# Optimization experiments

Hardware: AMD Instinct MI355X
Metric: run time of the kernel (lower is better)

The kernel has to match this reference:

```python
import jax, jax.numpy as jnp
import numpy as np

B, T, D, E = 2, 1653, 512, 8
D_E = D // E
BE = B * E


def setup_inputs() -> dict:
    key = jax.random.key(0)
    ks = jax.random.split(key, 11)
    s = 0.02  # keep linear-layer scale sane
    return {
        "input": jax.random.normal(ks[0], (B, T, D), jnp.float32),
        "Wq": jax.random.normal(ks[1], (D, D), jnp.float32) * s,
        "bq": jax.random.normal(ks[2], (D,), jnp.float32) * s,
        "Wk": jax.random.normal(ks[3], (D, D), jnp.float32) * s,
        "bk": jax.random.normal(ks[4], (D,), jnp.float32) * s,
        "Wv": jax.random.normal(ks[5], (D, D), jnp.float32) * s,
        "bv": jax.random.normal(ks[6], (D,), jnp.float32) * s,
        "Wo": jax.random.normal(ks[7], (D, D), jnp.float32) * s,
        "bo": jax.random.normal(ks[8], (D,), jnp.float32) * s,
        # random 'gaussian orthogonal punishment' matrix (diag(norms) @ blockwise-QR in torch; random here)
        "punish": jax.random.normal(ks[9], (T, T), jnp.float32) * (1.0 / np.sqrt(T)),
        # random tensor produced by torch.nn.init.orthogonal_(att_score) in the source
        "att_orth": jax.random.normal(ks[10], (BE, T, T), jnp.float32) * (1.0 / np.sqrt(T)),
    }


def _learnable_sigmoid(x):
    return 1.2 / (1.0 + jnp.exp(-1.6 * x))


def reference(input, Wq, bq, Wk, bk, Wv, bv, Wo, bo, punish, att_orth):
    # torch nn.Linear: y = x @ W^T + b
    def proj(W, b):
        # [B,T,D] -> permute(0,2,1) -> [B,D,T] -> reshape to [B*E, T, D_E]
        y = jnp.einsum('btd,ed->bte', input, W) + b
        return y.transpose(0, 2, 1).reshape(BE, T, D_E)

    Q = _learnable_sigmoid(proj(Wq, bq))            # [BE, T, D_E] (mask_q is all-ones => no-op)
    K = _learnable_sigmoid(proj(Wk, bk))            # [BE, T, D_E]
    V = proj(Wv, bv)                                # [BE, T, D_E]

    inv_sqrt_T = 1.0 / jnp.sqrt(jnp.float32(T))
    att = jnp.einsum('btd,bsd->bts', Q, K) * inv_sqrt_T  # [BE, T, T]

    # punishment: elementwise mul by broadcast punish matrix, then matmul with
    # the (transposed) random orthogonal tensor: att = (att * P) @ orth^T
    att = (att * punish[None, :, :]) @ att_orth.transpose(0, 2, 1)  # [BE, T, T]

    att = jnp.where(att == 0.0, jnp.float32(-2e20), att)  # masked_fill(att==0, -2e20)

    out = jnp.einsum('bts,bsd->btd', att, V)        # [BE, T, D_E]
    # permute(0,2,1) -> [BE, D_E, T] -> reshape [B, D, T] -> permute -> [B, T, D]
    out = out.transpose(0, 2, 1).reshape(B, D, T).transpose(0, 2, 1)
    return jnp.einsum('btd,ed->bte', out, Wo) + bo   # [B, T, D]
```

## Files before the change

### kernel.cpp

```cpp
#include <hip/hip_runtime.h>

#define TT 1653
#define DD 512
#define BB 2
#define DE 64
#define BEH 16
#define TTILES 26
#define TPAD 1664
#define SQN 26
#define NJC 4
#define MPSTRIDE TPAD

typedef __attribute__((ext_vector_type(8))) short bf16x8;
typedef __attribute__((ext_vector_type(4))) float f32x4;
typedef short bf16x8u __attribute__((ext_vector_type(8), aligned(4)));
typedef float f32x4u  __attribute__((ext_vector_type(4), aligned(4)));

__device__ __forceinline__ short f2bf(float f) {
    union { float f; unsigned u; } v; v.f = f;
    unsigned r = v.u + 0x7fffu + ((v.u >> 16) & 1u);
    return (short)(r >> 16);
}
__device__ __forceinline__ unsigned pack2(float a, float b) {
    return (unsigned)(unsigned short)f2bf(a) | ((unsigned)(unsigned short)f2bf(b) << 16);
}
__device__ __forceinline__ float bf2f(short s) {
    union { unsigned u; float f; } v; v.u = ((unsigned)(unsigned short)s) << 16;
    return v.f;
}
__device__ __forceinline__ bf16x8 ld_frag4(const short* p) {
    bf16x8u v = *(const bf16x8u*)p;
    return (bf16x8)v;
}

__device__ __forceinline__ void bar_fenced() {
    __builtin_amdgcn_sched_barrier(0);
    __builtin_amdgcn_s_barrier();
    __builtin_amdgcn_sched_barrier(0);
}
__device__ __forceinline__ void lgkm0_bar() {
    asm volatile("s_waitcnt lgkmcnt(0)" ::: "memory");
    __builtin_amdgcn_sched_barrier(0);
    __builtin_amdgcn_s_barrier();
    __builtin_amdgcn_sched_barrier(0);
}

__global__ __launch_bounds__(256) void projconv_kernel(
    const float* __restrict__ X,
    const float* __restrict__ W0, const float* __restrict__ b0,
    const float* __restrict__ W1, const float* __restrict__ b1,
    const float* __restrict__ W2, const float* __restrict__ b2,
    const float* __restrict__ P,
    short* __restrict__ Y0, short* __restrict__ Y1, short* __restrict__ Y2,
    short* __restrict__ Pbf)
{
    __shared__ __align__(16) short Wsh[64][72];
    __shared__ __align__(16) short Xs[64][72];

    const int tid = threadIdx.x;
    const int z = blockIdx.z;

    if (z == 6) {
        const int cid = blockIdx.x + TTILES * blockIdx.y;
        const int NG4 = TPAD / 4;
        for (int g = cid * 256 + tid; g < TT * NG4; g += 208 * 256) {
            const int r = g / NG4, c4 = (g - r * NG4) * 4;
            float p0 = 0.f, p1 = 0.f, p2 = 0.f, p3 = 0.f;
            const float* prow = P + (size_t)r * TT;
            if (c4 + 0 < TT) p0 = prow[c4 + 0];
            if (c4 + 1 < TT) p1 = prow[c4 + 1];
            if (c4 + 2 < TT) p2 = prow[c4 + 2];
            if (c4 + 3 < TT) p3 = prow[c4 + 3];
            uint2 o; o.x = pack2(p0, p1); o.y = pack2(p2, p3);
            *(uint2*)(Pbf + (size_t)r * TPAD + c4) = o;
        }
        return;
    }

    const int tt = blockIdx.x, dt = blockIdx.y;
    const int b = z / 3, which = z % 3;
    const float* W    = (which == 0) ? W0 : (which == 1) ? W1 : W2;
    const float* bias = (which == 0) ? b0 : (which == 1) ? b1 : b2;
    short* Y          = (which == 0) ? Y0 : (which == 1) ? Y1 : Y2;

    const int t0 = tt * 64, d0 = dt * 64;
    const float* Xb = X + (size_t)b * TT * DD;

    const int wave = tid >> 6, lane = tid & 63;
    const int quad = lane >> 4, l16 = lane & 15;
    const int srow = tid >> 2, scg = (tid & 3) * 16;
    const int trow = t0 + srow;
    const int rx = min(trow, TT - 1);

    f32x4 acc[4];
    #pragma unroll
    for (int i = 0; i < 4; ++i) acc[i] = (f32x4){0.f, 0.f, 0.f, 0.f};

    float4 w0, w1, w2, w3, x0, x1, x2, x3;

    auto stage = [&](int k0) {
        const float* wrow = W + (size_t)(d0 + srow) * DD + k0 + scg;
        w0 = *(const float4*)(wrow);
        w1 = *(const float4*)(wrow + 4);
        w2 = *(const float4*)(wrow + 8);
        w3 = *(const float4*)(wrow + 12);
        const float* xrow = Xb + (size_t)rx * DD + k0 + scg;
        x0 = *(const float4*)(xrow);
        x1 = *(const float4*)(xrow + 4);
        x2 = *(const float4*)(xrow + 8);
        x3 = *(const float4*)(xrow + 12);
    };
    auto lds_write = [&]() {
        const bool tv = (trow < TT);
        float4 zz = make_float4(0.f, 0.f, 0.f, 0.f);
        float4 y0 = tv ? x0 : zz, y1 = tv ? x1 : zz;
        float4 y2 = tv ? x2 : zz, y3 = tv ? x3 : zz;
        uint4 pw0, pw1, px0, px1;
        pw0.x = pack2(w0.x, w0.y); pw0.y = pack2(w0.z, w0.w);
        pw0.z = pack2(w1.x, w1.y); pw0.w = pack2(w1.z, w1.w);
        pw1.x = pack2(w2.x, w2.y); pw1.y = pack2(w2.z, w2.w);
        pw1.z = pack2(w3.x, w3.y); pw1.w = pack2(w3.z, w3.w);
        px0.x = pack2(y0.x, y0.y); px0.y = pack2(y0.z, y0.w);
        px0.z = pack2(y1.x, y1.y); px0.w = pack2(y1.z, y1.w);
        px1.x = pack2(y2.x, y2.y); px1.y = pack2(y2.z, y2.w);
        px1.z = pack2(y3.x, y3.y); px1.w = pack2(y3.z, y3.w);
        *(uint4*)&Wsh[srow][scg]     = pw0;
        *(uint4*)&Wsh[srow][scg + 8] = pw1;
        *(uint4*)&Xs[srow][scg]      = px0;
        *(uint4*)&Xs[srow][scg + 8]  = px1;
    };

    stage(0);
    for (int k0 = 0; k0 < DD; k0 += 64) {
        lds_write();
        if (k0 + 64 < DD) stage(k0 + 64);
        lgkm0_bar();

        #pragma unroll
        for (int ks = 0; ks < 2; ++ks) {
            bf16x8 a = *(const bf16x8*)&Wsh[wave * 16 + l16][ks * 32 + quad * 8];
            #pragma unroll
            for (int nt = 0; nt < 4; ++nt) {
                bf16x8 bb = *(const bf16x8*)&Xs[nt * 16 + l16][ks * 32 + quad * 8];
                acc[nt] = __builtin_amdgcn_mfma_f32_16x16x32_bf16(a, bb, acc[nt], 0, 0, 0);
            }
        }
        bar_fenced();
    }

    #pragma unroll
    for (int nt = 0; nt < 4; ++nt) {
        const int t = t0 + nt * 16 + l16;
        if (t < TT) {
            #pragma unroll
            for (int r = 0; r < 4; ++r) {
                const int d = d0 + wave * 16 + quad * 4 + r;
                float v = acc[nt][r] + bias[d];
                if (which < 2) v = 1.2f / (1.0f + __expf(-1.6f * v));
                Y[((size_t)b * DD + d) * TT + t] = f2bf(v);
            }
        }
    }
}

struct OVStage {
    f32x4u o0a, o0b, o1a, o1b;
    uint2  v0a, v0b, v1a, v1b;
};

__global__ __launch_bounds__(256) void ovt8_kernel(
    const float* __restrict__ orth, const short* __restrict__ Vb,
    float* __restrict__ Mpart)
{
    __shared__ __align__(16) short Os[64][70];
    __shared__ __align__(16) short Vs[64][70];

    const int flat = blockIdx.x + TTILES * (blockIdx.y + BEH * blockIdx.z);
    const int xcd = flat & 7;
    const int j8  = flat >> 3;
    const int sq  = j8 % 26;
    const int slice = xcd * 8 + (j8 / 26);
    const int be = slice & 15;
    const int jc = slice >> 4;

    const int s0 = sq * 64;
    const int jt0 = (jc < 2) ? jc * 7 : 14 + (jc - 2) * 6;
    const int jtn = (jc < 2) ? 7 : 6;

    const float* O  = orth + (size_t)be * TT * TT;
    const short* Vh = Vb + (size_t)be * DE * TT;

    const int tid  = threadIdx.x;
    const int wave = tid >> 6, lane = tid & 63;
    const int quad = lane >> 4, l16 = lane & 15;

    const int p  = tid >> 4;
    const int sc = tid & 15;
    const int ca = s0 + 4 * sc;
    const bool fastS = (s0 + 64 <= TT);

    f32x4 acc[4];
    #pragma unroll
    for (int i = 0; i < 4; ++i) acc[i] = (f32x4){0.f, 0.f, 0.f, 0.f};

    auto stage_load = [&](OVStage& S, int j0) {
        const int jA = j0 + 2 * p;
        const int r0  = min(jA,      TT - 1);
        const int r0b = min(jA + 1,  TT - 1);
        const int r1  = min(jA + 32, TT - 1);
        const int r1b = min(jA + 33, TT - 1);
        if (fastS) {
            S.o0a = *(const f32x4u*)(O + (size_t)r0  * TT + ca);
            S.o0b = *(const f32x4u*)(O + (size_t)r0b * TT + ca);
            S.o1a = *(const f32x4u*)(O + (size_t)r1  * TT + ca);
            S.o1b = *(const f32x4u*)(O + (size_t)r1b * TT + ca);
        } else {
            #pragma unroll
            for (int i = 0; i < 4; ++i) {
                const int col = ca + i;
                const bool cv = (col < TT);
                S.o0a[i] = cv ? O[(size_t)r0  * TT + col] : 0.f;
                S.o0b[i] = cv ? O[(size_t)r0b * TT + col] : 0.f;
                S.o1a[i] = cv ? O[(size_t)r1  * TT + col] : 0.f;
                S.o1b[i] = cv ? O[(size_t)r1b * TT + col] : 0.f;
            }
        }
        S.v0a = *(const uint2*)(Vh + (size_t)r0  * DE + 4 * sc);
        S.v0b = *(const uint2*)(Vh + (size_t)r0b * DE + 4 * sc);
        S.v1a = *(const uint2*)(Vh + (size_t)r1  * DE + 4 * sc);
        S.v1b = *(const uint2*)(Vh + (size_t)r1b * DE + 4 * sc);
    };

    auto lds_write = [&](const OVStage& S, int j0) {
        const int jA = j0 + 2 * p;
        #pragma unroll
        for (int i = 0; i < 4; ++i) {
            *(unsigned*)&Os[4 * sc + i][2 * p]      = pack2(S.o0a[i], S.o0b[i]);
            *(unsigned*)&Os[4 * sc + i][2 * p + 32] = pack2(S.o1a[i], S.o1b[i]);
        }
        const uint2 z = make_uint2(0u, 0u);
        uint2 v0a = (jA      < TT) ? S.v0a : z;
        uint2 v0b = (jA + 1  < TT) ? S.v0b : z;
        uint2 v1a = (jA + 32 < TT) ? S.v1a : z;
        uint2 v1b = (jA + 33 < TT) ? S.v1b : z;
        *(unsigned*)&Vs[4 * sc + 0][2 * p]      = (v0a.x & 0xffffu) | (v0b.x << 16);
        *(unsigned*)&Vs[4 * sc + 1][2 * p]      = (v0a.x >> 16)     | (v0b.x & 0xffff0000u);
        *(unsigned*)&Vs[4 * sc + 2][2 * p]      = (v0a.y & 0xffffu) | (v0b.y << 16);
        *(unsigned*)&Vs[4 * sc + 3][2 * p]      = (v0a.y >> 16)     | (v0b.y & 0xffff0000u);
        *(unsigned*)&Vs[4 * sc + 0][2 * p + 32] = (v1a.x & 0xffffu) | (v1b.x << 16);
        *(unsigned*)&Vs[4 * sc + 1][2 * p + 32] = (v1a.x >> 16)     | (v1b.x & 0xffff0000u);
        *(unsigned*)&Vs[4 * sc + 2][2 * p + 32] = (v1a.y & 0xffffu) | (v1b.y << 16);
        *(unsigned*)&Vs[4 * sc + 3][2 * p + 32] = (v1a.y >> 16)     | (v1b.y & 0xffff0000u);
    };

    auto mfma_tile = [&]() {
        #pragma unroll
        for (int ks = 0; ks < 2; ++ks) {
            bf16x8 bb = ld_frag4(&Os[wave * 16 + l16][ks * 32 + quad * 8]);
            #pragma unroll
            for (int i = 0; i < 4; ++i) {
                bf16x8 a = ld_frag4(&Vs[i * 16 + l16][ks * 32 + quad * 8]);
                acc[i] = __builtin_amdgcn_mfma_f32_16x16x32_bf16(a, bb, acc[i], 0, 0, 0);
            }
        }
    };

    OVStage sA, sB;
    stage_load(sA, (jt0 + 0) * 64);
    stage_load(sB, (jt0 + 1) * 64);

    for (int t = 0; t < jtn; t += 2) {
        lds_write(sA, (jt0 + t) * 64);
        if (t + 2 < jtn) stage_load(sA, (jt0 + t + 2) * 64);
        lgkm0_bar();
        mfma_tile();
        bar_fenced();
        if (t + 1 < jtn) {
            lds_write(sB, (jt0 + t + 1) * 64);
            if (t + 3 < jtn) stage_load(sB, (jt0 + t + 3) * 64);
            lgkm0_bar();
            mfma_tile();
            bar_fenced();
        }
    }

    float* Mp = Mpart + (size_t)(jc * BEH + be) * DE * MPSTRIDE;
    const int s = s0 + wave * 16 + l16;
    #pragma unroll
    for (int i = 0; i < 4; ++i) {
        #pragma unroll
        for (int r = 0; r < 4; ++r) {
            const int d = i * 16 + quad * 4 + r;
            Mp[(size_t)d * MPSTRIDE + s] = acc[i][r];
        }
    }
}

__global__ __launch_bounds__(256) void mreduce_kernel(
    const float* __restrict__ Mpart, short* __restrict__ Mt)
{
    const int g = blockIdx.x * 256 + threadIdx.x;
    const int NG = TPAD / 4;
    if (g >= BEH * DE * NG) return;
    const int bd = g / NG;
    const int s4 = (g - bd * NG) * 4;

    const size_t jstride = (size_t)BEH * DE * MPSTRIDE;
    const float* p = Mpart + (size_t)bd * MPSTRIDE + s4;
    float4 a0 = *(const float4*)(p);
    float4 a1 = *(const float4*)(p + jstride);
    float4 a2 = *(const float4*)(p + 2 * jstride);
    float4 a3 = *(const float4*)(p + 3 * jstride);
    float s0 = a0.x + a1.x + a2.x + a3.x;
    float s1 = a0.y + a1.y + a2.y + a3.y;
    float s2 = a0.z + a1.z + a2.z + a3.z;
    float s3 = a0.w + a1.w + a2.w + a3.w;

    uint2 o;
    o.x = pack2(s0, s1);
    o.y = pack2(s2, s3);
    *(uint2*)(Mt + (size_t)bd * TPAD + s4) = o;
}

struct AStage {
    uint4 k0, k1, m0, m1, p0, p1;
};

__global__ __launch_bounds__(256) void attn6_kernel(
    const short* __restrict__ Qb, const short* __restrict__ Kb,
    const short* __restrict__ Mt, const short* __restrict__ Pbf,
    float* __restrict__ Hbuf)
{
    __shared__ __align__(16) short Qs[64][72];
    __shared__ __align__(16) short Ks[64][72];
    __shared__ __align__(16) short Ms[64][72];
    __shared__ __align__(16) short Ps[64][72];

    const int flat = blockIdx.x + TTILES * blockIdx.y;
    const int xcd = flat & 7;
    const int j8  = flat >> 3;
    const int it  = j8 % 26;
    const int be  = xcd * 2 + (j8 / 26);

    const int b = be >> 3, e = be & 7;
    const int i0 = it * 64;
    const short* Qh = Qb + (size_t)be * DE * TT;
    const short* Kh = Kb + (size_t)be * DE * TT;
    const short* Mh = Mt + (size_t)be * DE * TPAD;

    const int tid  = threadIdx.x;
    const int wave = tid >> 6, lane = tid & 63;
    const int quad = lane >> 4, l16 = lane & 15;

    const float invs = 0.024598297f;

    const int srow = tid >> 2, scg = (tid & 3) * 16;
    const int gi = i0 + srow;
    const bool giv = (gi < TT);
    const int ri = min(gi, TT - 1);

    {
        uint4 z = make_uint4(0u, 0u, 0u, 0u);
        uint4 v0 = *(const uint4*)(Qh + (size_t)ri * DE + scg);
        uint4 v1 = *(const uint4*)(Qh + (size_t)ri * DE + scg + 8);
        if (!giv) { v0 = z; v1 = z; }
        *(uint4*)&Qs[srow][scg]     = v0;
        *(uint4*)&Qs[srow][scg + 8] = v1;
    }

    f32x4 out[4];
    #pragma unroll
    for (int i = 0; i < 4; ++i) out[i] = (f32x4){0.f, 0.f, 0.f, 0.f};

    auto stage_regs = [&](AStage& S, int s0) {
        const int gs = s0 + srow;
        const int rs = min(gs, TT - 1);
        S.k0 = *(const uint4*)(Kh + (size_t)rs * DE + scg);
        S.k1 = *(const uint4*)(Kh + (size_t)rs * DE + scg + 8);
        S.m0 = *(const uint4*)(Mh + (size_t)srow * TPAD + s0 + scg);
        S.m1 = *(const uint4*)(Mh + (size_t)srow * TPAD + s0 + scg + 8);
        S.p0 = *(const uint4*)(Pbf + (size_t)ri * TPAD + s0 + scg);
        S.p1 = *(const uint4*)(Pbf + (size_t)ri * TPAD + s0 + scg + 8);
    };

    auto lds_write = [&](const AStage& S, int s0) {
        const int gs = s0 + srow;
        const uint4 z = make_uint4(0u, 0u, 0u, 0u);
        const bool kv = (gs < TT);
        uint4 k0 = kv ? S.k0 : z, k1 = kv ? S.k1 : z;
        uint4 p0 = giv ? S.p0 : z, p1 = giv ? S.p1 : z;
        *(uint4*)&Ks[srow][scg]     = k0;
        *(uint4*)&Ks[srow][scg + 8] = k1;
        *(uint4*)&Ms[srow][scg]     = S.m0;
        *(uint4*)&Ms[srow][scg + 8] = S.m1;
        *(uint4*)&Ps[srow][scg]     = p0;
        *(uint4*)&Ps[srow][scg + 8] = p1;
    };

    auto compute = [&]() {
        f32x4 w[4];
        #pragma unroll
        for (int i = 0; i < 4; ++i) w[i] = (f32x4){0.f, 0.f, 0.f, 0.f};
        #pragma unroll
        for (int ks = 0; ks < 2; ++ks) {
            bf16x8 a = *(const bf16x8*)&Qs[wave * 16 + l16][ks * 32 + quad * 8];
            #pragma unroll
            for (int stile = 0; stile < 4; ++stile) {
                bf16x8 bb = *(const bf16x8*)&Ks[stile * 16 + l16][ks * 32 + quad * 8];
                w[stile] = __builtin_amdgcn_mfma_f32_16x16x32_bf16(a, bb, w[stile], 0, 0, 0);
            }
        }

        #pragma unroll
        for (int stile = 0; stile < 4; ++stile) {
            const int sl = stile * 16 + l16;
            #pragma unroll
            for (int r = 0; r < 4; ++r) {
                const int il = wave * 16 + quad * 4 + r;
                float v = w[stile][r] * invs * bf2f(Ps[il][sl]);
                Ps[il][sl] = f2bf(v);
            }
        }

        #pragma unroll
        for (int ks = 0; ks < 2; ++ks) {
            bf16x8 a = *(const bf16x8*)&Ps[wave * 16 + l16][ks * 32 + quad * 8];
            #pragma unroll
            for (int dt = 0; dt < 4; ++dt) {
                bf16x8 bb = *(const bf16x8*)&Ms[dt * 16 + l16][ks * 32 + quad * 8];
                out[dt] = __builtin_amdgcn_mfma_f32_16x16x32_bf16(a, bb, out[dt], 0, 0, 0);
            }
        }
    };

    AStage sA, sB;
    stage_regs(sA, 0);
    stage_regs(sB, 64);
    lgkm0_bar();

    for (int tt = 0; tt < TTILES; tt += 2) {
        lds_write(sA, tt * 64);
        if (tt + 2 < TTILES) stage_regs(sA, (tt + 2) * 64);
        lgkm0_bar();
        compute();
        bar_fenced();
        lds_write(sB, (tt + 1) * 64);
        if (tt + 3 < TTILES) stage_regs(sB, (tt + 3) * 64);
        lgkm0_bar();
        compute();
        bar_fenced();
    }

    #pragma unroll
    for (int dt = 0; dt < 4; ++dt) {
        const int d = dt * 16 + l16;
        #pragma unroll
        for (int r = 0; r < 4; ++r) {
            const int go = i0 + wave * 16 + quad * 4 + r;
            if (go < TT)
                Hbuf[((size_t)b * TT + go) * DD + e * 64 + d] = out[dt][r];
        }
    }
}

__global__ __launch_bounds__(256) void oproj_kernel(
    const float* __restrict__ H, const float* __restrict__ Wo,
    const float* __restrict__ bo, float* __restrict__ out)
{
    __shared__ float Hs[16][68];
    __shared__ float Ns[16][68];

    const int tt = blockIdx.x, nt = blockIdx.y, b = blockIdx.z;
    const int t0 = tt * 64, n0 = nt * 64;
    const float* Hb = H + (size_t)b * TT * DD;

    const int tid = threadIdx.x;
    const int tx = tid & 15, ty = tid >> 4;
    const int lrow = tid >> 2, lq = tid & 3;
    const int trow = t0 + lrow;

    float acc[4][4] = {};

    for (int k0 = 0; k0 < DD; k0 += 16) {
        float4 hv = make_float4(0.f, 0.f, 0.f, 0.f);
        if (trow < TT)
            hv = *(const float4*)(Hb + (size_t)trow * DD + k0 + lq*4);
        float4 wv = *(const float4*)(Wo + (size_t)(n0 + lrow) * DD + k0 + lq*4);
        __syncthreads();
        Hs[lq*4+0][lrow] = hv.x; Hs[lq*4+1][lrow] = hv.y;
        Hs[lq*4+2][lrow] = hv.z; Hs[lq*4+3][lrow] = hv.w;
        Ns[lq*4+0][lrow] = wv.x; Ns[lq*4+1][lrow] = wv.y;
        Ns[lq*4+2][lrow] = wv.z; Ns[lq*4+3][lrow] = wv.w;
        __syncthreads();
        #pragma unroll
        for (int k = 0; k < 16; ++k) {
            float4 a4 = *(const float4*)(&Hs[k][ty*4]);
            float4 c4 = *(const float4*)(&Ns[k][tx*4]);
            float a[4] = {a4.x, a4.y, a4.z, a4.w};
            float c[4] = {c4.x, c4.y, c4.z, c4.w};
            #pragma unroll
            for (int i = 0; i < 4; ++i)
                #pragma unroll
                for (int j = 0; j < 4; ++j)
                    acc[i][j] = fmaf(a[i], c[j], acc[i][j]);
        }
        __syncthreads();
    }

    #pragma unroll
    for (int i = 0; i < 4; ++i) {
        const int t = t0 + ty*4 + i;
        if (t < TT) {
            float4 v;
            v.x = acc[i][0] + bo[n0 + tx*4 + 0];
            v.y = acc[i][1] + bo[n0 + tx*4 + 1];
            v.z = acc[i][2] + bo[n0 + tx*4 + 2];
            v.w = acc[i][3] + bo[n0 + tx*4 + 3];
            *(float4*)(out + ((size_t)b * TT + t) * DD + n0 + tx*4) = v;
        }
    }
}

extern "C" void kernel_launch(void* const* d_in, const int* in_sizes, int n_in,
                              void* d_out, int out_size, void* d_ws, size_t ws_size,
                              hipStream_t stream)
{
    (void)in_sizes; (void)n_in; (void)out_size; (void)ws_size;

    const float* X    = (const float*)d_in[0];
    const float* Wq   = (const float*)d_in[1];
    const float* bq   = (const float*)d_in[2];
    const float* Wk   = (const float*)d_in[3];
    const float* bk   = (const float*)d_in[4];
    const float* Wv   = (const float*)d_in[5];
    const float* bv   = (const float*)d_in[6];
    const float* Wo   = (const float*)d_in[7];
    const float* bo   = (const float*)d_in[8];
    const float* P    = (const float*)d_in[9];
    const float* orth = (const float*)d_in[10];
    float* out = (float*)d_out;

    char* ws = (char*)d_ws;
    const size_t SZH = (size_t)BB * DD * TT * sizeof(short);
    short* Qb  = (short*)(ws);
    short* Kb  = (short*)(ws + SZH);
    short* Vb  = (short*)(ws + 2 * SZH);
    short* Mtb = (short*)(ws + 3 * SZH);
    short* Pbf = (short*)(ws + 3 * SZH + (size_t)BEH * DE * TPAD * sizeof(short));
    char*  after_p = ws + 3 * SZH + (size_t)BEH * DE * TPAD * sizeof(short)
                        + (size_t)TT * TPAD * sizeof(short);
    float* Mpart = (float*)after_p;
    float* Hbuf  = (float*)after_p;

    dim3 blk(256);

    dim3 g1(TTILES, DD / 64, BB * 3 + 1);
    projconv_kernel<<<g1, blk, 0, stream>>>(X, Wq, bq, Wk, bk, Wv, bv, P,
                                            Qb, Kb, Vb, Pbf);

    dim3 g2(SQN, BEH, NJC);
    ovt8_kernel<<<g2, blk, 0, stream>>>(orth, Vb, Mpart);

    dim3 gr((BEH * DE * (TPAD / 4) + 255) / 256);
    mreduce_kernel<<<gr, blk, 0, stream>>>(Mpart, Mtb);

    dim3 g3(TTILES, BEH);
    attn6_kernel<<<g3, blk, 0, stream>>>(Qb, Kb, Mtb, Pbf, Hbuf);

    dim3 g4(TTILES, DD / 64, BB);
    oproj_kernel<<<g4, blk, 0, stream>>>(Hbuf, Wo, bo, out);
}
```

Measured before the change: 408.3 us.

## Pre-convert X and QKV weights to bf16; double-buffer output projection LDS

A new prep kernel converts X, Wq, Wk, Wv and the punish matrix to bf16 once. The projection kernel then loads bf16 directly instead of re-reading and re-packing fp32 data in every tile. This halves global traffic in the projection GEMM and removes the repeated conversions, at the cost of an extra launch and an extra write-plus-read of X. Separately, the output projection gets double-buffered LDS with prefetch of the next k-slice, which drops one barrier per iteration.

```diff
diff --git a/kernel.cpp b/kernel.cpp
--- a/kernel.cpp
+++ b/kernel.cpp
@@ -45,26 +45,33 @@
     __builtin_amdgcn_sched_barrier(0);
 }
 
-__global__ __launch_bounds__(256) void projconv_kernel(
+__global__ __launch_bounds__(256) void prep_kernel(
     const float* __restrict__ X,
-    const float* __restrict__ W0, const float* __restrict__ b0,
-    const float* __restrict__ W1, const float* __restrict__ b1,
-    const float* __restrict__ W2, const float* __restrict__ b2,
-    const float* __restrict__ P,
-    short* __restrict__ Y0, short* __restrict__ Y1, short* __restrict__ Y2,
+    const float* __restrict__ Wq, const float* __restrict__ Wk,
+    const float* __restrict__ Wv, const float* __restrict__ P,
+    short* __restrict__ Xb16,
+    short* __restrict__ Wqb, short* __restrict__ Wkb, short* __restrict__ Wvb,
     short* __restrict__ Pbf)
 {
-    __shared__ __align__(16) short Wsh[64][72];
-    __shared__ __align__(16) short Xs[64][72];
-
-    const int tid = threadIdx.x;
-    const int z = blockIdx.z;
-
-    if (z == 6) {
-        const int cid = blockIdx.x + TTILES * blockIdx.y;
-        const int NG4 = TPAD / 4;
-        for (int g = cid * 256 + tid; g < TT * NG4; g += 208 * 256) {
-            const int r = g / NG4, c4 = (g - r * NG4) * 4;
+    const int NX4 = (BB * TT * DD) / 4;
+    const int NW4 = (DD * DD) / 4;
+    const int NP4 = TT * (TPAD / 4);
+    const int total = NX4 + 3 * NW4 + NP4;
+    const int stride = gridDim.x * 256;
+
+    for (int g = blockIdx.x * 256 + threadIdx.x; g < total; g += stride) {
+        if (g < NX4 + 3 * NW4) {
+            const float* src; short* dst; int idx4;
+            if (g < NX4)                { src = X;  dst = Xb16; idx4 = g; }
+            else if (g < NX4 + NW4)     { src = Wq; dst = Wqb;  idx4 = g - NX4; }
+            else if (g < NX4 + 2 * NW4) { src = Wk; dst = Wkb;  idx4 = g - NX4 - NW4; }
+            else                        { src = Wv; dst = Wvb;  idx4 = g - NX4 - 2 * NW4; }
+            float4 a = *(const float4*)(src + (size_t)idx4 * 4);
+            uint2 o; o.x = pack2(a.x, a.y); o.y = pack2(a.z, a.w);
+            *(uint2*)(dst + (size_t)idx4 * 4) = o;
+        } else {
+            const int gp = g - (NX4 + 3 * NW4);
+            const int r = gp / (TPAD / 4), c4 = (gp - r * (TPAD / 4)) * 4;
             float p0 = 0.f, p1 = 0.f, p2 = 0.f, p3 = 0.f;
             const float* prow = P + (size_t)r * TT;
             if (c4 + 0 < TT) p0 = prow[c4 + 0];
@@ -74,18 +81,29 @@
             uint2 o; o.x = pack2(p0, p1); o.y = pack2(p2, p3);
             *(uint2*)(Pbf + (size_t)r * TPAD + c4) = o;
         }
-        return;
-    }
-
-    const int tt = blockIdx.x, dt = blockIdx.y;
+    }
+}
+
+__global__ __launch_bounds__(256) void proj7_kernel(
+    const short* __restrict__ Xb16,
+    const short* __restrict__ W0b, const float* __restrict__ b0,
+    const short* __restrict__ W1b, const float* __restrict__ b1,
+    const short* __restrict__ W2b, const float* __restrict__ b2,
+    short* __restrict__ Y0, short* __restrict__ Y1, short* __restrict__ Y2)
+{
+    __shared__ __align__(16) short Wsh[64][72];
+    __shared__ __align__(16) short Xs[64][72];
+
+    const int tt = blockIdx.x, dt = blockIdx.y, z = blockIdx.z;
     const int b = z / 3, which = z % 3;
-    const float* W    = (which == 0) ? W0 : (which == 1) ? W1 : W2;
+    const short* W    = (which == 0) ? W0b : (which == 1) ? W1b : W2b;
     const float* bias = (which == 0) ? b0 : (which == 1) ? b1 : b2;
     short* Y          = (which == 0) ? Y0 : (which == 1) ? Y1 : Y2;
 
     const int t0 = tt * 64, d0 = dt * 64;
-    const float* Xb = X + (size_t)b * TT * DD;
-
+    const short* Xb = Xb16 + (size_t)b * TT * DD;
+
+    const int tid  = threadIdx.x;
     const int wave = tid >> 6, lane = tid & 63;
     const int quad = lane >> 4, l16 = lane & 15;
     const int srow = tid >> 2, scg = (tid & 3) * 16;
@@ -96,38 +114,24 @@
     #pragma unroll
     for (int i = 0; i < 4; ++i) acc[i] = (f32x4){0.f, 0.f, 0.f, 0.f};
 
-    float4 w0, w1, w2, w3, x0, x1, x2, x3;
+    uint4 wlo, whi, xlo, xhi;
 
     auto stage = [&](int k0) {
-        const float* wrow = W + (size_t)(d0 + srow) * DD + k0 + scg;
-        w0 = *(const float4*)(wrow);
-        w1 = *(const float4*)(wrow + 4);
-        w2 = *(const float4*)(wrow + 8);
-        w3 = *(const float4*)(wrow + 12);
-        const float* xrow = Xb + (size_t)rx * DD + k0 + scg;
-        x0 = *(const float4*)(xrow);
-        x1 = *(const float4*)(xrow + 4);
-        x2 = *(const float4*)(xrow + 8);
-        x3 = *(const float4*)(xrow + 12);
+        const short* wrow = W + (size_t)(d0 + srow) * DD + k0 + scg;
+        wlo = *(const uint4*)(wrow);
+        whi = *(const uint4*)(wrow + 8);
+        const short* xrow = Xb + (size_t)rx * DD + k0 + scg;
+        xlo = *(const uint4*)(xrow);
+        xhi = *(const uint4*)(xrow + 8);
     };
     auto lds_write = [&]() {
+        const uint4 z4 = make_uint4(0u, 0u, 0u, 0u);
         const bool tv = (trow < TT);
-        float4 zz = make_float4(0.f, 0.f, 0.f, 0.f);
-        float4 y0 = tv ? x0 : zz, y1 = tv ? x1 : zz;
-        float4 y2 = tv ? x2 : zz, y3 = tv ? x3 : zz;
-        uint4 pw0, pw1, px0, px1;
-        pw0.x = pack2(w0.x, w0.y); pw0.y = pack2(w0.z, w0.w);
-        pw0.z = pack2(w1.x, w1.y); pw0.w = pack2(w1.z, w1.w);
-        pw1.x = pack2(w2.x, w2.y); pw1.y = pack2(w2.z, w2.w);
-        pw1.z = pack2(w3.x, w3.y); pw1.w = pack2(w3.z, w3.w);
-        px0.x = pack2(y0.x, y0.y); px0.y = pack2(y0.z, y0.w);
-        px0.z = pack2(y1.x, y1.y); px0.w = pack2(y1.z, y1.w);
-        px1.x = pack2(y2.x, y2.y); px1.y = pack2(y2.z, y2.w);
-        px1.z = pack2(y3.x, y3.y); px1.w = pack2(y3.z, y3.w);
-        *(uint4*)&Wsh[srow][scg]     = pw0;
-        *(uint4*)&Wsh[srow][scg + 8] = pw1;
-        *(uint4*)&Xs[srow][scg]      = px0;
-        *(uint4*)&Xs[srow][scg + 8]  = px1;
+        uint4 y0 = tv ? xlo : z4, y1 = tv ? xhi : z4;
+        *(uint4*)&Wsh[srow][scg]     = wlo;
+        *(uint4*)&Wsh[srow][scg + 8] = whi;
+        *(uint4*)&Xs[srow][scg]      = y0;
+        *(uint4*)&Xs[srow][scg + 8]  = y1;
     };
 
     stage(0);
@@ -463,12 +467,12 @@
     }
 }
 
-__global__ __launch_bounds__(256) void oproj_kernel(
+__global__ __launch_bounds__(256) void oproj3_kernel(
     const float* __restrict__ H, const float* __restrict__ Wo,
     const float* __restrict__ bo, float* __restrict__ out)
 {
-    __shared__ float Hs[16][68];
-    __shared__ float Ns[16][68];
+    __shared__ float Hs[2][16][68];
+    __shared__ float Ns[2][16][68];
 
     const int tt = blockIdx.x, nt = blockIdx.y, b = blockIdx.z;
     const int t0 = tt * 64, n0 = nt * 64;
@@ -478,24 +482,33 @@
     const int tx = tid & 15, ty = tid >> 4;
     const int lrow = tid >> 2, lq = tid & 3;
     const int trow = t0 + lrow;
+    const int rx = min(trow, TT - 1);
 
     float acc[4][4] = {};
-
-    for (int k0 = 0; k0 < DD; k0 += 16) {
-        float4 hv = make_float4(0.f, 0.f, 0.f, 0.f);
-        if (trow < TT)
-            hv = *(const float4*)(Hb + (size_t)trow * DD + k0 + lq*4);
-        float4 wv = *(const float4*)(Wo + (size_t)(n0 + lrow) * DD + k0 + lq*4);
-        __syncthreads();
-        Hs[lq*4+0][lrow] = hv.x; Hs[lq*4+1][lrow] = hv.y;
-        Hs[lq*4+2][lrow] = hv.z; Hs[lq*4+3][lrow] = hv.w;
-        Ns[lq*4+0][lrow] = wv.x; Ns[lq*4+1][lrow] = wv.y;
-        Ns[lq*4+2][lrow] = wv.z; Ns[lq*4+3][lrow] = wv.w;
-        __syncthreads();
+    float4 hv, wv;
+
+    auto stage = [&](int k0) {
+        hv = *(const float4*)(Hb + (size_t)rx * DD + k0 + lq * 4);
+        wv = *(const float4*)(Wo + (size_t)(n0 + lrow) * DD + k0 + lq * 4);
+    };
+    auto lds_write = [&](int buf) {
+        float4 h2 = (trow < TT) ? hv : make_float4(0.f, 0.f, 0.f, 0.f);
+        Hs[buf][lq*4+0][lrow] = h2.x; Hs[buf][lq*4+1][lrow] = h2.y;
+        Hs[buf][lq*4+2][lrow] = h2.z; Hs[buf][lq*4+3][lrow] = h2.w;
+        Ns[buf][lq*4+0][lrow] = wv.x; Ns[buf][lq*4+1][lrow] = wv.y;
+        Ns[buf][lq*4+2][lrow] = wv.z; Ns[buf][lq*4+3][lrow] = wv.w;
+    };
+
+    stage(0);
+    lds_write(0);
+    for (int it = 0; it < 32; ++it) {
+        lgkm0_bar();
+        if (it + 1 < 32) stage((it + 1) * 16);
+        const int cur = it & 1;
         #pragma unroll
         for (int k = 0; k < 16; ++k) {
-            float4 a4 = *(const float4*)(&Hs[k][ty*4]);
-            float4 c4 = *(const float4*)(&Ns[k][tx*4]);
+            float4 a4 = *(const float4*)(&Hs[cur][k][ty*4]);
+            float4 c4 = *(const float4*)(&Ns[cur][k][tx*4]);
             float a[4] = {a4.x, a4.y, a4.z, a4.w};
             float c[4] = {c4.x, c4.y, c4.z, c4.w};
             #pragma unroll
@@ -504,7 +517,7 @@
                 for (int j = 0; j < 4; ++j)
                     acc[i][j] = fmaf(a[i], c[j], acc[i][j]);
         }
-        __syncthreads();
+        if (it + 1 < 32) lds_write((it + 1) & 1);
     }
 
     #pragma unroll
@@ -542,21 +555,30 @@
 
     char* ws = (char*)d_ws;
     const size_t SZH = (size_t)BB * DD * TT * sizeof(short);
-    short* Qb  = (short*)(ws);
-    short* Kb  = (short*)(ws + SZH);
-    short* Vb  = (short*)(ws + 2 * SZH);
-    short* Mtb = (short*)(ws + 3 * SZH);
-    short* Pbf = (short*)(ws + 3 * SZH + (size_t)BEH * DE * TPAD * sizeof(short));
-    char*  after_p = ws + 3 * SZH + (size_t)BEH * DE * TPAD * sizeof(short)
-                        + (size_t)TT * TPAD * sizeof(short);
-    float* Mpart = (float*)after_p;
-    float* Hbuf  = (float*)after_p;
+    const size_t SZMT = (size_t)BEH * DE * TPAD * sizeof(short);
+    const size_t SZP  = (size_t)TT * TPAD * sizeof(short);
+    const size_t SZW  = (size_t)DD * DD * sizeof(short);
+    short* Qb   = (short*)(ws);
+    short* Kb   = (short*)(ws + SZH);
+    short* Vb   = (short*)(ws + 2 * SZH);
+    short* Mtb  = (short*)(ws + 3 * SZH);
+    short* Pbf  = (short*)(ws + 3 * SZH + SZMT);
+    short* Xb16 = (short*)(ws + 3 * SZH + SZMT + SZP);
+    short* Wqb  = (short*)(ws + 4 * SZH + SZMT + SZP);
+    short* Wkb  = (short*)(ws + 4 * SZH + SZMT + SZP + SZW);
+    short* Wvb  = (short*)(ws + 4 * SZH + SZMT + SZP + 2 * SZW);
+    char*  after = ws + 4 * SZH + SZMT + SZP + 3 * SZW;
+    float* Mpart = (float*)after;
+    float* Hbuf  = (float*)after;
 
     dim3 blk(256);
 
-    dim3 g1(TTILES, DD / 64, BB * 3 + 1);
-    projconv_kernel<<<g1, blk, 0, stream>>>(X, Wq, bq, Wk, bk, Wv, bv, P,
-                                            Qb, Kb, Vb, Pbf);
+    prep_kernel<<<dim3(1024), blk, 0, stream>>>(X, Wq, Wk, Wv, P,
+                                                Xb16, Wqb, Wkb, Wvb, Pbf);
+
+    dim3 g1(TTILES, DD / 64, BB * 3);
+    proj7_kernel<<<g1, blk, 0, stream>>>(Xb16, Wqb, bq, Wkb, bk, Wvb, bv,
+                                         Qb, Kb, Vb);
 
     dim3 g2(SQN, BEH, NJC);
     ovt8_kernel<<<g2, blk, 0, stream>>>(orth, Vb, Mpart);
@@ -568,5 +590,5 @@
     attn6_kernel<<<g3, blk, 0, stream>>>(Qb, Kb, Mtb, Pbf, Hbuf);
 
     dim3 g4(TTILES, DD / 64, BB);
-    oproj_kernel<<<g4, blk, 0, stream>>>(Hbuf, Wo, bo, out);
-}
+    oproj3_kernel<<<g4, blk, 0, stream>>>(Hbuf, Wo, bo, out);
+}
```

After: 390.9 us. 1.04x faster.
